# Performance work log

Hardware: AMD Instinct MI355X
Metric: run time of the kernel (lower is better)

## Reference

```python
import jax, jax.numpy as jnp
import numpy as np

OUT_FEATURES = 11008  # LLaMA-7B FFN intermediate
IN_FEATURES = 4096    # d_model
N_TOKENS = 16         # small M -> weight-traffic bound
SCALE = 0.01
ZERO_POINT = 0


def setup_inputs() -> dict:
    key = jax.random.key(0)
    k1, k2 = jax.random.split(key)
    x = jax.random.normal(k1, (N_TOKENS, IN_FEATURES), dtype=jnp.float32)
    weight_int8 = jax.random.randint(
        k2, (OUT_FEATURES, IN_FEATURES), -128, 128, dtype=jnp.int32
    ).astype(jnp.int8)
    return {
        "x": x,
        "weight_int8": weight_int8,
        "scale": SCALE,
        "zero_point": ZERO_POINT,
    }


def reference(x, weight_int8, scale, zero_point):
    # Dequantize INT8 weight to fp32 (same elementwise pass as the torch module)
    weight_fp = (weight_int8.astype(jnp.float32) - zero_point) * scale  # [out, in]
    # F.linear(x, W) == x @ W.T
    return jnp.einsum("ti,oi->to", x, weight_fp)
```

## Files before the change

kernel.cpp:

```cpp
#include <hip/hip_runtime.h>
#include <hip/hip_bf16.h>
#include <stdint.h>


#define M_TOK 16
#define K_DIM 4096
#define N_OUT 11008

typedef int v4i __attribute__((ext_vector_type(4)));

__global__ __launch_bounds__(256) void quant_x_kernel(
    const float* __restrict__ x, int8_t* __restrict__ xh,
    int8_t* __restrict__ xl, float* __restrict__ s1_out,
    float* __restrict__ sumx_out) {
  const int t = blockIdx.x;
  const int tid = threadIdx.x;
  const float4* xv = (const float4*)(x + (long)t * K_DIM) + tid * 4;

  float vals[16];
  float m = 0.0f, s = 0.0f;
#pragma unroll
  for (int j = 0; j < 4; ++j) {
    float4 f = xv[j];
    vals[j * 4 + 0] = f.x; vals[j * 4 + 1] = f.y;
    vals[j * 4 + 2] = f.z; vals[j * 4 + 3] = f.w;
    m = fmaxf(m, fmaxf(fmaxf(fabsf(f.x), fabsf(f.y)),
                       fmaxf(fabsf(f.z), fabsf(f.w))));
    s += f.x + f.y + f.z + f.w;
  }
#pragma unroll
  for (int off = 32; off > 0; off >>= 1) {
    m = fmaxf(m, __shfl_xor(m, off));
    s += __shfl_xor(s, off);
  }
  __shared__ float lm[4], ls[4];
  const int w = tid >> 6;
  if ((tid & 63) == 0) { lm[w] = m; ls[w] = s; }
  __syncthreads();
  m = fmaxf(fmaxf(lm[0], lm[1]), fmaxf(lm[2], lm[3]));
  s = ls[0] + ls[1] + ls[2] + ls[3];

  const float s1 = (m > 0.0f) ? (m * (1.0f / 127.0f)) : 1.0f;
  const float inv = 1.0f / s1;
  if (tid == 0) { s1_out[t] = s1; sumx_out[t] = s; }

  int hq[16], lq[16];
#pragma unroll
  for (int j = 0; j < 16; ++j) {
    float xf = vals[j];
    float h = rintf(xf * inv);
    h = fminf(fmaxf(h, -127.0f), 127.0f);
    float resid = xf - h * s1;
    float l = rintf(resid * inv * 256.0f);
    l = fminf(fmaxf(l, -128.0f), 127.0f);
    hq[j] = (int)h;
    lq[j] = (int)l;
  }
  int4 hv, lv;
  int* hp = (int*)&hv;
  int* lp = (int*)&lv;
#pragma unroll
  for (int d = 0; d < 4; ++d) {
    uint32_t hw = 0, lw = 0;
#pragma unroll
    for (int j = 0; j < 4; ++j) {
      hw |= (uint32_t)(hq[d * 4 + j] & 0xff) << (8 * j);
      lw |= (uint32_t)(lq[d * 4 + j] & 0xff) << (8 * j);
    }
    hp[d] = (int)hw;
    lp[d] = (int)lw;
  }
  ((int4*)xh)[(long)t * 256 + tid] = hv;
  ((int4*)xl)[(long)t * 256 + tid] = lv;
}

__global__ __launch_bounds__(256) void qgemm_kernel(
    const int* __restrict__ W, const int8_t* __restrict__ xh,
    const int8_t* __restrict__ xl, const float* __restrict__ s1,
    const float* __restrict__ sumx, const float* __restrict__ scale_p,
    const int* __restrict__ zp_p, float* __restrict__ out) {
  const int tid = threadIdx.x;
  const int lane = tid & 63;
  const int w = tid >> 6;
  const int obase = blockIdx.x * 16;
  const int n = lane & 15;
  const int g = lane >> 4;
  const long kbase = (long)w * 1024 + g * 16;

  const int* Wp = W + (long)(obase + n) * K_DIM + kbase;
  const v4i* Ah = (const v4i*)(xh + (long)n * K_DIM + kbase);
  const v4i* Al = (const v4i*)(xl + (long)n * K_DIM + kbase);

  v4i accH = {0, 0, 0, 0};
  v4i accL = {0, 0, 0, 0};
#pragma unroll 4
  for (int c = 0; c < 16; ++c) {
    const int4* wq = (const int4*)(Wp + c * 64);
    v4i b;
#pragma unroll
    for (int d = 0; d < 4; ++d) {
      int4 q = wq[d];
      uint32_t packed = ((uint32_t)q.x & 0xffu) |
                        (((uint32_t)q.y & 0xffu) << 8) |
                        (((uint32_t)q.z & 0xffu) << 16) |
                        (((uint32_t)q.w & 0xffu) << 24);
      b[d] = (int)packed;
    }
    v4i ah = Ah[c * 4];
    v4i al = Al[c * 4];
    accH = __builtin_amdgcn_mfma_i32_16x16x64_i8(ah, b, accH, 0, 0, 0);
    accL = __builtin_amdgcn_mfma_i32_16x16x64_i8(al, b, accL, 0, 0, 0);
  }

  __shared__ float red[4][16 * 17];
#pragma unroll
  for (int r = 0; r < 4; ++r) {
    float f = (float)accH[r] + (float)accL[r] * (1.0f / 256.0f);
    int t = g * 4 + r;
    red[w][t * 17 + n] = f;
  }
  __syncthreads();

  const int t = tid >> 4;
  const int col = tid & 15;
  float sum = red[0][t * 17 + col] + red[1][t * 17 + col] +
              red[2][t * 17 + col] + red[3][t * 17 + col];
  const float sc = scale_p[0];
  const float zp = (float)zp_p[0];
  float o = sc * (s1[t] * sum) - sc * zp * sumx[t];
  out[(long)t * N_OUT + obase + col] = o;
}

extern "C" void kernel_launch(void* const* d_in, const int* in_sizes, int n_in,
                              void* d_out, int out_size, void* d_ws,
                              size_t ws_size, hipStream_t stream) {
  const float* x = (const float*)d_in[0];
  const int* Wq = (const int*)d_in[1];
  const float* scale_p = (const float*)d_in[2];
  const int* zp_p = (const int*)d_in[3];
  float* out = (float*)d_out;

  int8_t* xh = (int8_t*)d_ws;
  int8_t* xl = xh + (long)M_TOK * K_DIM;
  float* s1 = (float*)(xl + (long)M_TOK * K_DIM);
  float* sumx = s1 + M_TOK;

  quant_x_kernel<<<M_TOK, 256, 0, stream>>>(x, xh, xl, s1, sumx);
  qgemm_kernel<<<N_OUT / 16, 256, 0, stream>>>(Wq, xh, xl, s1, sumx, scale_p,
                                               zp_p, out);
}
```

Before: 256.9 us.

## Split K across four blocks with atomic output accumulation and nontemporal weight loads

The GEMM grid grows fourfold by splitting the K dimension into four chunks, each handled by a separate block, with partial results combined through float atomicAdd into an output that the quantize kernel now zeroes first. Weight loads switch to nontemporal loads. The aim is more waves in flight to saturate HBM bandwidth on the weight stream, which is int32-stored and large. In exchange it adds atomic traffic, zeroing writes, and nondeterministic float summation order.

New measurement: 272.4 us. 1.06x slower.

```diff
diff --git a/kernel.cpp b/kernel.cpp
--- a/kernel.cpp
+++ b/kernel.cpp
@@ -12,9 +12,21 @@
 __global__ __launch_bounds__(256) void quant_x_kernel(
     const float* __restrict__ x, int8_t* __restrict__ xh,
     int8_t* __restrict__ xl, float* __restrict__ s1_out,
-    float* __restrict__ sumx_out) {
+    float* __restrict__ sumx_out, float* __restrict__ out) {
   const int t = blockIdx.x;
   const int tid = threadIdx.x;
+
+  {
+    float4* o4 = (float4*)out;
+    const int gidx = blockIdx.x * 256 + tid;
+    const float4 z = {0.f, 0.f, 0.f, 0.f};
+#pragma unroll
+    for (int i = 0; i < 11; ++i) {
+      int idx = gidx + i * 4096;
+      if (idx < (M_TOK * N_OUT) / 4) o4[idx] = z;
+    }
+  }
+
   const float4* xv = (const float4*)(x + (long)t * K_DIM) + tid * 4;
 
   float vals[16];
@@ -82,10 +94,11 @@
   const int tid = threadIdx.x;
   const int lane = tid & 63;
   const int w = tid >> 6;
-  const int obase = blockIdx.x * 16;
+  const int kidx = blockIdx.x & 3;
+  const int obase = (blockIdx.x >> 2) * 16;
   const int n = lane & 15;
   const int g = lane >> 4;
-  const long kbase = (long)w * 1024 + g * 16;
+  const long kbase = (long)kidx * 1024 + w * 256 + g * 16;
 
   const int* Wp = W + (long)(obase + n) * K_DIM + kbase;
   const v4i* Ah = (const v4i*)(xh + (long)n * K_DIM + kbase);
@@ -93,13 +106,13 @@
 
   v4i accH = {0, 0, 0, 0};
   v4i accL = {0, 0, 0, 0};
-#pragma unroll 4
-  for (int c = 0; c < 16; ++c) {
-    const int4* wq = (const int4*)(Wp + c * 64);
+#pragma unroll
+  for (int c = 0; c < 4; ++c) {
+    const v4i* wq = (const v4i*)(Wp + c * 64);
     v4i b;
 #pragma unroll
     for (int d = 0; d < 4; ++d) {
-      int4 q = wq[d];
+      v4i q = __builtin_nontemporal_load(wq + d);
       uint32_t packed = ((uint32_t)q.x & 0xffu) |
                         (((uint32_t)q.y & 0xffu) << 8) |
                         (((uint32_t)q.z & 0xffu) << 16) |
@@ -126,9 +139,12 @@
   float sum = red[0][t * 17 + col] + red[1][t * 17 + col] +
               red[2][t * 17 + col] + red[3][t * 17 + col];
   const float sc = scale_p[0];
-  const float zp = (float)zp_p[0];
-  float o = sc * (s1[t] * sum) - sc * zp * sumx[t];
-  out[(long)t * N_OUT + obase + col] = o;
+  float o = sc * (s1[t] * sum);
+  if (kidx == 0) {
+    const float zp = (float)zp_p[0];
+    o -= sc * zp * sumx[t];
+  }
+  atomicAdd(&out[(long)t * N_OUT + obase + col], o);
 }
 
 extern "C" void kernel_launch(void* const* d_in, const int* in_sizes, int n_in,
@@ -145,7 +161,7 @@
   float* s1 = (float*)(xl + (long)M_TOK * K_DIM);
   float* sumx = s1 + M_TOK;
 
-  quant_x_kernel<<<M_TOK, 256, 0, stream>>>(x, xh, xl, s1, sumx);
-  qgemm_kernel<<<N_OUT / 16, 256, 0, stream>>>(Wq, xh, xl, s1, sumx, scale_p,
-                                               zp_p, out);
+  quant_x_kernel<<<M_TOK, 256, 0, stream>>>(x, xh, xl, s1, sumx, out);
+  qgemm_kernel<<<(N_OUT / 16) * 4, 256, 0, stream>>>(Wq, xh, xl, s1, sumx,
+                                                     scale_p, zp_p, out);
 }
```

## Load weight rows coalesced per wave and transpose through swizzled LDS with prefetch

Applied to the files above, without the earlier changes.

Each wave now reads four whole weight rows with contiguous 16-byte-per-lane loads, instead of each lane striding across 16 rows. The int32 values are packed to int8 and staged in a double-buffered, XOR-swizzled shared memory tile, which lanes read back in MFMA operand layout. The next chunk's global loads are issued into registers one iteration ahead to overlap latency. The cost is a block-wide barrier every iteration, plus extra LDS traffic and register pressure.

After: 254.0 us. About the same (-1.1%).

```diff
diff --git a/kernel.cpp b/kernel.cpp
--- a/kernel.cpp
+++ b/kernel.cpp
@@ -85,49 +85,77 @@
   const int obase = blockIdx.x * 16;
   const int n = lane & 15;
   const int g = lane >> 4;
-  const long kbase = (long)w * 1024 + g * 16;
+  const int r0 = w * 4;
 
-  const int* Wp = W + (long)(obase + n) * K_DIM + kbase;
-  const v4i* Ah = (const v4i*)(xh + (long)n * K_DIM + kbase);
-  const v4i* Al = (const v4i*)(xl + (long)n * K_DIM + kbase);
+  __shared__ v4i wbuf[2][256];
+  __shared__ float red[4][16 * 17];
+
+  const v4i* Wr0 = (const v4i*)(W + (long)(obase + r0 + 0) * K_DIM) + lane;
+  const v4i* Wr1 = (const v4i*)(W + (long)(obase + r0 + 1) * K_DIM) + lane;
+  const v4i* Wr2 = (const v4i*)(W + (long)(obase + r0 + 2) * K_DIM) + lane;
+  const v4i* Wr3 = (const v4i*)(W + (long)(obase + r0 + 3) * K_DIM) + lane;
+
+  int wr_idx[4];
+#pragma unroll
+  for (int r = 0; r < 4; ++r) {
+    const int row = r0 + r;
+    wr_idx[r] = row * 64 + (lane ^ ((row & 7) << 2));
+  }
+  const int rd_idx = n * 16 + ((4 * w + g) ^ (n & 7));
+
+  const v4i* Ah = (const v4i*)xh + (n * 256 + w * 4 + g);
+  const v4i* Al = (const v4i*)xl + (n * 256 + w * 4 + g);
+
+  v4i wreg[2][4];
+  wreg[0][0] = Wr0[0];
+  wreg[0][1] = Wr1[0];
+  wreg[0][2] = Wr2[0];
+  wreg[0][3] = Wr3[0];
 
   v4i accH = {0, 0, 0, 0};
   v4i accL = {0, 0, 0, 0};
-#pragma unroll 4
+
+#pragma unroll
   for (int c = 0; c < 16; ++c) {
-    const int4* wq = (const int4*)(Wp + c * 64);
-    v4i b;
+    const int cur = c & 1;
+    if (c + 1 < 16) {
+      const int nxt = (c + 1) & 1;
+      wreg[nxt][0] = Wr0[(c + 1) * 64];
+      wreg[nxt][1] = Wr1[(c + 1) * 64];
+      wreg[nxt][2] = Wr2[(c + 1) * 64];
+      wreg[nxt][3] = Wr3[(c + 1) * 64];
+    }
+    uint32_t* wb = (uint32_t*)wbuf[cur];
 #pragma unroll
-    for (int d = 0; d < 4; ++d) {
-      int4 q = wq[d];
+    for (int r = 0; r < 4; ++r) {
+      v4i q = wreg[cur][r];
       uint32_t packed = ((uint32_t)q.x & 0xffu) |
                         (((uint32_t)q.y & 0xffu) << 8) |
                         (((uint32_t)q.z & 0xffu) << 16) |
                         (((uint32_t)q.w & 0xffu) << 24);
-      b[d] = (int)packed;
+      wb[wr_idx[r]] = packed;
     }
-    v4i ah = Ah[c * 4];
-    v4i al = Al[c * 4];
-    accH = __builtin_amdgcn_mfma_i32_16x16x64_i8(ah, b, accH, 0, 0, 0);
-    accL = __builtin_amdgcn_mfma_i32_16x16x64_i8(al, b, accL, 0, 0, 0);
+    __syncthreads();
+    const v4i b = wbuf[cur][rd_idx];
+    accH = __builtin_amdgcn_mfma_i32_16x16x64_i8(Ah[c * 16], b, accH, 0, 0, 0);
+    accL = __builtin_amdgcn_mfma_i32_16x16x64_i8(Al[c * 16], b, accL, 0, 0, 0);
   }
 
-  __shared__ float red[4][16 * 17];
 #pragma unroll
   for (int r = 0; r < 4; ++r) {
     float f = (float)accH[r] + (float)accL[r] * (1.0f / 256.0f);
-    int t = g * 4 + r;
+    const int t = g * 4 + r;
     red[w][t * 17 + n] = f;
   }
   __syncthreads();
 
   const int t = tid >> 4;
   const int col = tid & 15;
-  float sum = red[0][t * 17 + col] + red[1][t * 17 + col] +
-              red[2][t * 17 + col] + red[3][t * 17 + col];
+  const float sum = red[0][t * 17 + col] + red[1][t * 17 + col] +
+                    red[2][t * 17 + col] + red[3][t * 17 + col];
   const float sc = scale_p[0];
   const float zp = (float)zp_p[0];
-  float o = sc * (s1[t] * sum) - sc * zp * sumx[t];
+  const float o = sc * (s1[t] * sum) - sc * zp * sumx[t];
   out[(long)t * N_OUT + obase + col] = o;
 }
 
```

## Stage weight slab through LDS with fully coalesced global loads and XOR swizzle

Applied to the files above, without the earlier changes.

Each block now loads its 16-row weight slab (stored as int32 per element) with fully coalesced contiguous v4i loads across all threads, packs the values to int8, and writes them into a 64KB XOR-swizzled LDS buffer. MFMA operands are then read from LDS instead of from strided per-lane global loads. This targets poor coalescing in the weight stream, which dominates traffic. The cost is 64KB+ of shared memory per block, which limits occupancy, and a full barrier that serialises the load and compute phases.

Result: slower. 266.9 us (+3.9%).

```diff
diff --git a/kernel.cpp b/kernel.cpp
--- a/kernel.cpp
+++ b/kernel.cpp
@@ -85,49 +85,60 @@
   const int obase = blockIdx.x * 16;
   const int n = lane & 15;
   const int g = lane >> 4;
-  const long kbase = (long)w * 1024 + g * 16;
 
-  const int* Wp = W + (long)(obase + n) * K_DIM + kbase;
-  const v4i* Ah = (const v4i*)(xh + (long)n * K_DIM + kbase);
-  const v4i* Al = (const v4i*)(xl + (long)n * K_DIM + kbase);
+  __shared__ uint32_t wbuf[16 * 1024];
+  __shared__ float red[4][16 * 17];
 
+  const v4i* slab = (const v4i*)(W + (long)obase * K_DIM);
+#pragma unroll
+  for (int b = 0; b < 16; ++b) {
+    v4i q0 = slab[(b * 4 + 0) * 256 + tid];
+    v4i q1 = slab[(b * 4 + 1) * 256 + tid];
+    v4i q2 = slab[(b * 4 + 2) * 256 + tid];
+    v4i q3 = slab[(b * 4 + 3) * 256 + tid];
+#pragma unroll
+    for (int u = 0; u < 4; ++u) {
+      v4i q = (u == 0) ? q0 : (u == 1) ? q1 : (u == 2) ? q2 : q3;
+      const int idx = (b * 4 + u) * 256 + tid;
+      const int row = idx >> 10;
+      const int k4 = idx & 1023;
+      uint32_t p = ((uint32_t)q.x & 0xffu) |
+                   (((uint32_t)q.y & 0xffu) << 8) |
+                   (((uint32_t)q.z & 0xffu) << 16) |
+                   (((uint32_t)q.w & 0xffu) << 24);
+      const int wr = (row << 10) | (((k4 >> 2) ^ (row & 7)) << 2) | (k4 & 3);
+      wbuf[wr] = p;
+    }
+  }
+  __syncthreads();
+
+  const v4i* Ah = (const v4i*)xh + n * 256 + w * 64 + g;
+  const v4i* Al = (const v4i*)xl + n * 256 + w * 64 + g;
   v4i accH = {0, 0, 0, 0};
   v4i accL = {0, 0, 0, 0};
-#pragma unroll 4
-  for (int c = 0; c < 16; ++c) {
-    const int4* wq = (const int4*)(Wp + c * 64);
-    v4i b;
 #pragma unroll
-    for (int d = 0; d < 4; ++d) {
-      int4 q = wq[d];
-      uint32_t packed = ((uint32_t)q.x & 0xffu) |
-                        (((uint32_t)q.y & 0xffu) << 8) |
-                        (((uint32_t)q.z & 0xffu) << 16) |
-                        (((uint32_t)q.w & 0xffu) << 24);
-      b[d] = (int)packed;
-    }
-    v4i ah = Ah[c * 4];
-    v4i al = Al[c * 4];
-    accH = __builtin_amdgcn_mfma_i32_16x16x64_i8(ah, b, accH, 0, 0, 0);
-    accL = __builtin_amdgcn_mfma_i32_16x16x64_i8(al, b, accL, 0, 0, 0);
+  for (int it = 0; it < 16; ++it) {
+    const int j = w * 64 + it * 4 + g;
+    const v4i b = *(const v4i*)&wbuf[(n << 10) | ((j ^ (n & 7)) << 2)];
+    accH = __builtin_amdgcn_mfma_i32_16x16x64_i8(Ah[it * 4], b, accH, 0, 0, 0);
+    accL = __builtin_amdgcn_mfma_i32_16x16x64_i8(Al[it * 4], b, accL, 0, 0, 0);
   }
 
-  __shared__ float red[4][16 * 17];
 #pragma unroll
   for (int r = 0; r < 4; ++r) {
     float f = (float)accH[r] + (float)accL[r] * (1.0f / 256.0f);
-    int t = g * 4 + r;
+    const int t = g * 4 + r;
     red[w][t * 17 + n] = f;
   }
   __syncthreads();
 
   const int t = tid >> 4;
   const int col = tid & 15;
-  float sum = red[0][t * 17 + col] + red[1][t * 17 + col] +
-              red[2][t * 17 + col] + red[3][t * 17 + col];
+  const float sum = red[0][t * 17 + col] + red[1][t * 17 + col] +
+                    red[2][t * 17 + col] + red[3][t * 17 + col];
   const float sc = scale_p[0];
   const float zp = (float)zp_p[0];
-  float o = sc * (s1[t] * sum) - sc * zp * sumx[t];
+  const float o = sc * (s1[t] * sum) - sc * zp * sumx[t];
   out[(long)t * N_OUT + obase + col] = o;
 }
 
```
